# Kernel optimization log

Hardware: AMD Instinct MI355X
Metric: run time of the kernel (lower is better)

## Reference

```python
import jax, jax.numpy as jnp
import numpy as np

N = 8_000_000

def _rotation_matrix(weight):
    # weight: [3,1] Euler angles (a=roll/x, b=pitch/y, c=yaw/z), ZYX intrinsic
    a, b, c = weight[0, 0], weight[1, 0], weight[2, 0]
    sa, ca = jnp.sin(a), jnp.cos(a)
    sb, cb = jnp.sin(b), jnp.cos(b)
    sc, cc = jnp.sin(c), jnp.cos(c)
    R = jnp.stack([
        jnp.stack([cc * cb, sa * sb * cc - ca * sc, ca * sb * cc + sa * sc]),
        jnp.stack([cb * sc, sa * sb * sc + ca * cc, ca * sb * sc - sa * cc]),
        jnp.stack([-sb,     sa * cb,                ca * cb]),
    ])  # [3,3]
    return R

def setup_inputs() -> dict:
    key = jax.random.key(0)
    k1, k2 = jax.random.split(key)
    x = jax.random.normal(k1, (N, 3), dtype=jnp.float32)
    weight = jax.random.normal(k2, (3, 1), dtype=jnp.float32)
    return {"x": x, "weight": weight}

def reference(x, weight):
    # z[i] = R @ x[i]  ->  z = x @ R^T, computed once (loop in original is constant R)
    R = _rotation_matrix(weight)
    return x @ R.T  # [N,3]
```

## Files before the change

### kernel.cpp

```cpp
#include <hip/hip_runtime.h>
#include <math.h>


__global__ __launch_bounds__(256) void rot_apply_kernel(
    const float* __restrict__ x,
    const float* __restrict__ w,
    float* __restrict__ out,
    long long n_groups)
{
    __shared__ float Rs[9];
    if (threadIdx.x == 0) {
        float a = w[0], b = w[1], c = w[2];
        float sa, ca, sb, cb, sc, cc;
        sincosf(a, &sa, &ca);
        sincosf(b, &sb, &cb);
        sincosf(c, &sc, &cc);
        Rs[0] = cc * cb;
        Rs[1] = sa * sb * cc - ca * sc;
        Rs[2] = ca * sb * cc + sa * sc;
        Rs[3] = cb * sc;
        Rs[4] = sa * sb * sc + ca * cc;
        Rs[5] = ca * sb * sc - sa * cc;
        Rs[6] = -sb;
        Rs[7] = sa * cb;
        Rs[8] = ca * cb;
    }
    __syncthreads();
    const float R00 = Rs[0], R01 = Rs[1], R02 = Rs[2];
    const float R10 = Rs[3], R11 = Rs[4], R12 = Rs[5];
    const float R20 = Rs[6], R21 = Rs[7], R22 = Rs[8];

    const float4* __restrict__ x4 = (const float4*)x;
    float4* __restrict__ o4 = (float4*)out;

    const long long stride = (long long)gridDim.x * blockDim.x;
    for (long long g = (long long)blockIdx.x * blockDim.x + threadIdx.x;
         g < n_groups; g += stride) {
        const long long base = 3ll * g;
        float4 v0 = x4[base + 0];
        float4 v1 = x4[base + 1];
        float4 v2 = x4[base + 2];

        float px0 = v0.x, py0 = v0.y, pz0 = v0.z;
        float px1 = v0.w, py1 = v1.x, pz1 = v1.y;
        float px2 = v1.z, py2 = v1.w, pz2 = v2.x;
        float px3 = v2.y, py3 = v2.z, pz3 = v2.w;

        float a0 = fmaf(R00, px0, fmaf(R01, py0, R02 * pz0));
        float b0 = fmaf(R10, px0, fmaf(R11, py0, R12 * pz0));
        float c0 = fmaf(R20, px0, fmaf(R21, py0, R22 * pz0));

        float a1 = fmaf(R00, px1, fmaf(R01, py1, R02 * pz1));
        float b1 = fmaf(R10, px1, fmaf(R11, py1, R12 * pz1));
        float c1 = fmaf(R20, px1, fmaf(R21, py1, R22 * pz1));

        float a2 = fmaf(R00, px2, fmaf(R01, py2, R02 * pz2));
        float b2 = fmaf(R10, px2, fmaf(R11, py2, R12 * pz2));
        float c2 = fmaf(R20, px2, fmaf(R21, py2, R22 * pz2));

        float a3 = fmaf(R00, px3, fmaf(R01, py3, R02 * pz3));
        float b3 = fmaf(R10, px3, fmaf(R11, py3, R12 * pz3));
        float c3 = fmaf(R20, px3, fmaf(R21, py3, R22 * pz3));

        float4 w0, w1, w2;
        w0.x = a0; w0.y = b0; w0.z = c0; w0.w = a1;
        w1.x = b1; w1.y = c1; w1.z = a2; w1.w = b2;
        w2.x = c2; w2.y = a3; w2.z = b3; w2.w = c3;

        o4[base + 0] = w0;
        o4[base + 1] = w1;
        o4[base + 2] = w2;
    }
}

extern "C" void kernel_launch(void* const* d_in, const int* in_sizes, int n_in,
                              void* d_out, int out_size, void* d_ws, size_t ws_size,
                              hipStream_t stream) {
    const float* x = (const float*)d_in[0];
    const float* w = (const float*)d_in[1];
    float* out = (float*)d_out;

    const long long n_floats = (long long)in_sizes[0];
    const long long n_groups = n_floats / 12;

    const int block = 256;
    int grid = 2048;
    long long needed = (n_groups + block - 1) / block;
    if (needed < grid) grid = (int)needed;

    rot_apply_kernel<<<grid, block, 0, stream>>>(x, w, out, n_groups);
}
```

Baseline: 174.7 us.

## Stage float4 tiles through LDS for fully coalesced loads and stores

Each block now loads a tile of 768 float4 values with consecutive threads reading consecutive float4s, stages them in shared memory, and has each thread read its three float4s (four points) from LDS. Results are written back to LDS and then stored to global memory the same coalesced way. The grid-stride loop is replaced by one tile per block, which launches many more blocks. The aim is fully contiguous per-instruction global access in place of a stride-3 float4 pattern. The cost is extra LDS traffic, two barriers per block, a per-block sincos of R, and possible LDS bank conflicts on the strided 3*t accesses.

```diff
diff --git a/kernel.cpp b/kernel.cpp
--- a/kernel.cpp
+++ b/kernel.cpp
@@ -2,14 +2,22 @@
 #include <math.h>
 
 
-__global__ __launch_bounds__(256) void rot_apply_kernel(
+#define BLOCK 256
+#define TILE_F4 (BLOCK * 3)
+
+__global__ __launch_bounds__(BLOCK) void rot_apply_lds_kernel(
     const float* __restrict__ x,
     const float* __restrict__ w,
     float* __restrict__ out,
-    long long n_groups)
+    long long n4)
 {
+    __shared__ float4 s_in[TILE_F4];
+    __shared__ float4 s_out[TILE_F4];
     __shared__ float Rs[9];
-    if (threadIdx.x == 0) {
+
+    const int t = threadIdx.x;
+
+    if (t == 0) {
         float a = w[0], b = w[1], c = w[2];
         float sa, ca, sb, cb, sc, cc;
         sincosf(a, &sa, &ca);
@@ -25,51 +33,62 @@
         Rs[7] = sa * cb;
         Rs[8] = ca * cb;
     }
+
+    const float4* __restrict__ x4 = (const float4*)x;
+    float4* __restrict__ o4 = (float4*)out;
+
+    const long long tileBase = (long long)blockIdx.x * TILE_F4;
+
+#pragma unroll
+    for (int k = 0; k < 3; ++k) {
+        long long gi = tileBase + (long long)k * BLOCK + t;
+        if (gi < n4) s_in[k * BLOCK + t] = x4[gi];
+    }
     __syncthreads();
+
     const float R00 = Rs[0], R01 = Rs[1], R02 = Rs[2];
     const float R10 = Rs[3], R11 = Rs[4], R12 = Rs[5];
     const float R20 = Rs[6], R21 = Rs[7], R22 = Rs[8];
 
-    const float4* __restrict__ x4 = (const float4*)x;
-    float4* __restrict__ o4 = (float4*)out;
+    float4 v0 = s_in[3 * t + 0];
+    float4 v1 = s_in[3 * t + 1];
+    float4 v2 = s_in[3 * t + 2];
 
-    const long long stride = (long long)gridDim.x * blockDim.x;
-    for (long long g = (long long)blockIdx.x * blockDim.x + threadIdx.x;
-         g < n_groups; g += stride) {
-        const long long base = 3ll * g;
-        float4 v0 = x4[base + 0];
-        float4 v1 = x4[base + 1];
-        float4 v2 = x4[base + 2];
+    float px0 = v0.x, py0 = v0.y, pz0 = v0.z;
+    float px1 = v0.w, py1 = v1.x, pz1 = v1.y;
+    float px2 = v1.z, py2 = v1.w, pz2 = v2.x;
+    float px3 = v2.y, py3 = v2.z, pz3 = v2.w;
 
-        float px0 = v0.x, py0 = v0.y, pz0 = v0.z;
-        float px1 = v0.w, py1 = v1.x, pz1 = v1.y;
-        float px2 = v1.z, py2 = v1.w, pz2 = v2.x;
-        float px3 = v2.y, py3 = v2.z, pz3 = v2.w;
+    float a0 = fmaf(R00, px0, fmaf(R01, py0, R02 * pz0));
+    float b0 = fmaf(R10, px0, fmaf(R11, py0, R12 * pz0));
+    float c0 = fmaf(R20, px0, fmaf(R21, py0, R22 * pz0));
 
-        float a0 = fmaf(R00, px0, fmaf(R01, py0, R02 * pz0));
-        float b0 = fmaf(R10, px0, fmaf(R11, py0, R12 * pz0));
-        float c0 = fmaf(R20, px0, fmaf(R21, py0, R22 * pz0));
+    float a1 = fmaf(R00, px1, fmaf(R01, py1, R02 * pz1));
+    float b1 = fmaf(R10, px1, fmaf(R11, py1, R12 * pz1));
+    float c1 = fmaf(R20, px1, fmaf(R21, py1, R22 * pz1));
 
-        float a1 = fmaf(R00, px1, fmaf(R01, py1, R02 * pz1));
-        float b1 = fmaf(R10, px1, fmaf(R11, py1, R12 * pz1));
-        float c1 = fmaf(R20, px1, fmaf(R21, py1, R22 * pz1));
+    float a2 = fmaf(R00, px2, fmaf(R01, py2, R02 * pz2));
+    float b2 = fmaf(R10, px2, fmaf(R11, py2, R12 * pz2));
+    float c2 = fmaf(R20, px2, fmaf(R21, py2, R22 * pz2));
 
-        float a2 = fmaf(R00, px2, fmaf(R01, py2, R02 * pz2));
-        float b2 = fmaf(R10, px2, fmaf(R11, py2, R12 * pz2));
-        float c2 = fmaf(R20, px2, fmaf(R21, py2, R22 * pz2));
+    float a3 = fmaf(R00, px3, fmaf(R01, py3, R02 * pz3));
+    float b3 = fmaf(R10, px3, fmaf(R11, py3, R12 * pz3));
+    float c3 = fmaf(R20, px3, fmaf(R21, py3, R22 * pz3));
 
-        float a3 = fmaf(R00, px3, fmaf(R01, py3, R02 * pz3));
-        float b3 = fmaf(R10, px3, fmaf(R11, py3, R12 * pz3));
-        float c3 = fmaf(R20, px3, fmaf(R21, py3, R22 * pz3));
+    float4 w0, w1, w2;
+    w0.x = a0; w0.y = b0; w0.z = c0; w0.w = a1;
+    w1.x = b1; w1.y = c1; w1.z = a2; w1.w = b2;
+    w2.x = c2; w2.y = a3; w2.z = b3; w2.w = c3;
 
-        float4 w0, w1, w2;
-        w0.x = a0; w0.y = b0; w0.z = c0; w0.w = a1;
-        w1.x = b1; w1.y = c1; w1.z = a2; w1.w = b2;
-        w2.x = c2; w2.y = a3; w2.z = b3; w2.w = c3;
+    s_out[3 * t + 0] = w0;
+    s_out[3 * t + 1] = w1;
+    s_out[3 * t + 2] = w2;
+    __syncthreads();
 
-        o4[base + 0] = w0;
-        o4[base + 1] = w1;
-        o4[base + 2] = w2;
+#pragma unroll
+    for (int k = 0; k < 3; ++k) {
+        long long gi = tileBase + (long long)k * BLOCK + t;
+        if (gi < n4) o4[gi] = s_out[k * BLOCK + t];
     }
 }
 
@@ -81,12 +100,9 @@
     float* out = (float*)d_out;
 
     const long long n_floats = (long long)in_sizes[0];
-    const long long n_groups = n_floats / 12;
+    const long long n4 = n_floats / 4;
 
-    const int block = 256;
-    int grid = 2048;
-    long long needed = (n_groups + block - 1) / block;
-    if (needed < grid) grid = (int)needed;
+    const long long grid = (n4 + TILE_F4 - 1) / TILE_F4;
 
-    rot_apply_kernel<<<grid, block, 0, stream>>>(x, w, out, n_groups);
+    rot_apply_lds_kernel<<<(int)grid, BLOCK, 0, stream>>>(x, w, out, n4);
 }
```

After: 171.7 us. Within noise of the previous version (-1.7%).
